# Performance work log

Measured on AMD Instinct MI355X. Metric: run time of the kernel, lower is better.

Reference implementation:

```python
import jax, jax.numpy as jnp
import numpy as np

N = 50000
E = 800000
F = 64
HID = 64
HEADS = 4
NTYPES = 3


def layer_norm(x, g, b, eps=1e-5):
    mu = x.mean(-1, keepdims=True)
    var = ((x - mu) ** 2).mean(-1, keepdims=True)
    return (x - mu) * jax.lax.rsqrt(var + eps) * g + b


def gat_conv(x, src, dst, n, W, att_src, att_dst, bias, concat):
    # PyG GATConv: per-head linear transform, additive attention, segment softmax over dst.
    H, C = att_src.shape
    xp = (x @ W).reshape(n, H, C)                       # [N,H,C]
    a_s = (xp * att_src).sum(-1)                         # [N,H]
    a_d = (xp * att_dst).sum(-1)                         # [N,H]
    e = jax.nn.leaky_relu(a_s[src] + a_d[dst], 0.2)      # [Etot,H]
    m = jax.ops.segment_max(e, dst, num_segments=n)      # stable softmax per target
    ex = jnp.exp(e - m[dst])
    denom = jax.ops.segment_sum(ex, dst, num_segments=n)
    alpha = ex / (denom[dst] + 1e-16)                    # [Etot,H]
    msg = xp[src] * alpha[:, :, None]                    # [Etot,H,C]
    out = jax.ops.segment_sum(msg, dst, num_segments=n)  # [N,H,C]
    out = out.reshape(n, H * C) if concat else out.mean(1)
    return out + bias


def setup_inputs() -> dict:
    key = jax.random.key(0)
    ks = jax.random.split(key, 12)
    f32 = jnp.float32
    return {
        'node_features': jax.random.normal(ks[0], (N, F), f32),
        'node_types': jax.random.randint(ks[1], (N,), 0, NTYPES),
        'edge_index': jax.random.randint(ks[2], (2, E), 0, N),
        'type_emb': jax.random.normal(ks[3], (NTYPES, HID), f32) * 0.02,
        'proj_W': jax.random.normal(ks[4], (F, HID), f32) / np.sqrt(F).astype(np.float32),
        'proj_b': jnp.zeros((HID,), f32),
        'W0': jax.random.normal(ks[5], (HID, HEADS * HID), f32) / np.sqrt(HID).astype(np.float32),
        'att_src0': jax.random.normal(ks[6], (HEADS, HID), f32) * 0.1,
        'att_dst0': jax.random.normal(ks[7], (HEADS, HID), f32) * 0.1,
        'bias0': jnp.zeros((HEADS * HID,), f32),
        'ln0_g': jnp.ones((HEADS * HID,), f32),
        'ln0_b': jnp.zeros((HEADS * HID,), f32),
        'W1': jax.random.normal(ks[8], (HEADS * HID, HEADS * HID), f32) / np.sqrt(HEADS * HID).astype(np.float32),
        'att_src1': jax.random.normal(ks[9], (HEADS, HID), f32) * 0.1,
        'att_dst1': jax.random.normal(ks[10], (HEADS, HID), f32) * 0.1,
        'bias1': jnp.zeros((HID,), f32),
        'ln1_g': jnp.ones((HID,), f32),
        'ln1_b': jnp.zeros((HID,), f32),
    }


def reference(node_features, node_types, edge_index, type_emb, proj_W, proj_b,
              W0, att_src0, att_dst0, bias0, ln0_g, ln0_b,
              W1, att_src1, att_dst1, bias1, ln1_g, ln1_b):
    n = node_features.shape[0]
    loop = jnp.arange(n)
    src = jnp.concatenate([edge_index[0], loop])  # add_self_loops=True (PyG default)
    dst = jnp.concatenate([edge_index[1], loop])
    # input projection + node-type embedding
    x = node_features @ proj_W + proj_b + type_emb[node_types]
    # layer 0: concat heads -> [N, HEADS*HID]
    h = gat_conv(x, src, dst, n, W0, att_src0, att_dst0, bias0, True)
    h = jax.nn.relu(layer_norm(h, ln0_g, ln0_b))  # dropout is identity in eval
    # layer 1: mean over heads -> [N, HID]; residual skipped (shape mismatch 256 vs 64)
    h2 = gat_conv(h, src, dst, n, W1, att_src1, att_dst1, bias1, False)
    h2 = jax.nn.relu(layer_norm(h2, ln1_g, ln1_b))
    return h2
```

## Files before the change

### kernel.cpp

```cpp
#include <hip/hip_runtime.h>
#include <hip/hip_bf16.h>
#include <hip/hip_fp16.h>

typedef unsigned short u16;
typedef unsigned int u32;
typedef short s16x8 __attribute__((ext_vector_type(8)));
typedef float f32x4 __attribute__((ext_vector_type(4)));

__device__ __forceinline__ float bf2f(u16 u) {
  return __uint_as_float(((u32)u) << 16);
}

__device__ __forceinline__ u16 f2b(float f) {
  __hip_bfloat16 h = __float2bfloat16(f);
  return *(u16*)&h;
}

__device__ __forceinline__ u32 packbf(float lo, float hi) {
  return (u32)f2b(lo) | ((u32)f2b(hi) << 16);
}

__device__ __forceinline__ bool sniff_bf16(const void* ones) {
  u32 w = *(const u32*)ones;
  return (w >> 16) == (w & 0xFFFFu);
}

__device__ __forceinline__ float ldf(const void* p, size_t i, bool bf) {
  return bf ? bf2f(((const u16*)p)[i]) : ((const float*)p)[i];
}

__global__ __launch_bounds__(256) void deg_count_k(const int* __restrict__ ei, int E, int N,
                                                   int* __restrict__ deg) {
  int i = blockIdx.x * 256 + threadIdx.x;
  if (i >= E + N) return;
  int d = (i < E) ? ei[E + i] : (i - E);
  atomicAdd(deg + d, 1);
}

__global__ __launch_bounds__(256) void scan_local_k(const int* __restrict__ deg,
                                                    int* __restrict__ off,
                                                    int* __restrict__ bsum, int N) {
  __shared__ int ps[256];
  int t = threadIdx.x;
  int i = blockIdx.x * 256 + t;
  int v = (i < N) ? deg[i] : 0;
  ps[t] = v;
  __syncthreads();
#pragma unroll
  for (int o = 1; o < 256; o <<= 1) {
    int u = (t >= o) ? ps[t - o] : 0;
    __syncthreads();
    ps[t] += u;
    __syncthreads();
  }
  if (i < N) off[i] = ps[t] - v;
  if (t == 255) bsum[blockIdx.x] = ps[255];
}

__global__ __launch_bounds__(256) void scan_add2_k(int* __restrict__ off,
                                                   const int* __restrict__ bsum,
                                                   int* __restrict__ cur,
                                                   int N, int Etot, int nb) {
  __shared__ int red[256];
  int t = threadIdx.x;
  int b = blockIdx.x;
  red[t] = (t < nb && t < b) ? bsum[t] : 0;
  __syncthreads();
#pragma unroll
  for (int o = 128; o > 0; o >>= 1) {
    if (t < o) red[t] += red[t + o];
    __syncthreads();
  }
  int pre = red[0];
  int i = b * 256 + t;
  if (i == 0) off[N] = Etot;
  if (i >= N) return;
  int o2 = off[i] + pre;
  off[i] = o2;
  cur[i] = o2;
}

__global__ __launch_bounds__(256) void scatter_k(const int* __restrict__ ei, int E, int N,
                                                 int* __restrict__ cur, int* __restrict__ csr) {
  int i = blockIdx.x * 256 + threadIdx.x;
  if (i >= E + N) return;
  int s, d;
  if (i < E) { s = ei[i]; d = ei[E + i]; } else { s = i - E; d = s; }
  int p = atomicAdd(cur + d, 1);
  csr[p] = s;
}

__global__ __launch_bounds__(256) void prep_k(
    const void* __restrict__ W0, const void* __restrict__ W1,
    const void* __restrict__ pW, const void* __restrict__ atts,
    const void* __restrict__ attd, const void* __restrict__ pb,
    const void* __restrict__ temb, const void* __restrict__ ones,
    u16* __restrict__ Wp0, u16* __restrict__ Wp1, u16* __restrict__ Wpp,
    u16* __restrict__ Wpe, float* __restrict__ ca) {
  bool bf = sniff_bf16(ones);
  int b = blockIdx.x;
  int t = threadIdx.x;
  if (b < 320) {
    const void* W = (b < 64) ? W0 : W1;
    u16* Wp = (b < 64) ? Wp0 : Wp1;
    int i = (b < 64 ? b : b - 64) * 256 + t;
    int j = i & 7;
    int q = (i >> 3) & 3;
    int c = (i >> 5) & 255;
    int kc = i >> 13;
    int k = kc * 32 + q * 8 + j;
    Wp[i] = f2b(ldf(W, (size_t)k * 256 + c, bf));
  } else if (b < 336) {
    int i = (b - 320) * 256 + t;
    int j = i & 7;
    int q = (i >> 3) & 3;
    int c = (i >> 5) & 63;
    int kc = i >> 11;
    int k = kc * 32 + q * 8 + j;
    Wpp[i] = f2b(ldf(pW, (size_t)k * 64 + c, bf));
  } else {
    __shared__ float va[256], vd[256];
    int h = t >> 6, k = t & 63;
    {
      float s = 0.f, d = 0.f;
      for (int c = 0; c < 64; c++) {
        float w = ldf(W0, (size_t)k * 256 + h * 64 + c, bf);
        s += w * ldf(atts, h * 64 + c, bf);
        d += w * ldf(attd, h * 64 + c, bf);
      }
      va[t] = s;
      vd[t] = d;
    }
    __syncthreads();
    {
      int i = k;
      float wa = 0.f, wd = 0.f;
      for (int kk = 0; kk < 64; kk++) {
        float wv = ldf(pW, (size_t)i * 64 + kk, bf);
        wa += wv * va[h * 64 + kk];
        wd += wv * vd[h * 64 + kk];
      }
      int kc = i >> 5, q = (i >> 3) & 3, j = i & 7;
      Wpe[((kc * 16 + h) * 4 + q) * 8 + j] = f2b(wa);
      Wpe[((kc * 16 + 4 + h) * 4 + q) * 8 + j] = f2b(wd);
    }
    Wpe[256 + t] = 0;
    Wpe[768 + t] = 0;
    if (t < 12) {
      int ty = t >> 2, hh = t & 3;
      float sa = 0.f, sd = 0.f;
      for (int kk = 0; kk < 64; kk++) {
        float bv = ldf(pb, kk, bf) + ldf(temb, ty * 64 + kk, bf);
        sa += bv * va[hh * 64 + kk];
        sd += bv * vd[hh * 64 + kk];
      }
      ca[t] = sa;
      ca[12 + t] = sd;
    }
  }
}

__global__ __launch_bounds__(256) void proj2_k(
    const void* __restrict__ nf, const int* __restrict__ ntype,
    const u16* __restrict__ Wpp, const u16* __restrict__ Wpe,
    const void* __restrict__ pbias, const void* __restrict__ temb,
    const float* __restrict__ ca, const void* __restrict__ ones,
    u16* __restrict__ x, float* __restrict__ aS, float* __restrict__ aD, int N) {
  bool bf = sniff_bf16(ones);
  int t = threadIdx.x;
  int wave = t >> 6, lane = t & 63;
  int r = lane & 15, q = lane >> 4;
  int row0 = blockIdx.x * 16;
  int arow = row0 + r;
  if (arow >= N) arow = N - 1;
  f32x4 xacc = {0.f, 0.f, 0.f, 0.f};
  f32x4 eacc = {0.f, 0.f, 0.f, 0.f};
#pragma unroll
  for (int kc = 0; kc < 2; kc++) {
    s16x8 a;
    if (bf) {
      a = *(const s16x8*)((const u16*)nf + (size_t)arow * 64 + kc * 32 + q * 8);
    } else {
      const float* fp = (const float*)nf + (size_t)arow * 64 + kc * 32 + q * 8;
#pragma unroll
      for (int j = 0; j < 8; j++) a[j] = (short)f2b(fp[j]);
    }
    {
      int c = wave * 16 + r;
      s16x8 b = *(const s16x8*)(Wpp + (((size_t)kc * 64 + c) * 4 + q) * 8);
      xacc = __builtin_amdgcn_mfma_f32_16x16x32_bf16(a, b, xacc, 0, 0, 0);
    }
    if (wave == 3) {
      s16x8 b = *(const s16x8*)(Wpe + (((size_t)kc * 16 + r) * 4 + q) * 8);
      eacc = __builtin_amdgcn_mfma_f32_16x16x32_bf16(a, b, eacc, 0, 0, 0);
    }
  }
#pragma unroll
  for (int rg = 0; rg < 4; rg++) {
    int row = row0 + q * 4 + rg;
    if (row >= N) continue;
    int col = wave * 16 + r;
    int ty = ntype[row];
    float v = xacc[rg] + ldf(pbias, col, bf) + ldf(temb, ty * 64 + col, bf);
    x[(size_t)row * 64 + col] = f2b(v);
    if (wave == 3 && r < 8) {
      if (r < 4) aS[(size_t)row * 4 + r] = eacc[rg] + ca[ty * 4 + r];
      else       aD[(size_t)row * 4 + (r - 4)] = eacc[rg] + ca[12 + ty * 4 + (r - 4)];
    }
  }
}

__global__ __launch_bounds__(256) void agg0_k(
    const int* __restrict__ off, const int* __restrict__ csr,
    const float* __restrict__ aS, const float* __restrict__ aD,
    const u16* __restrict__ x, u16* __restrict__ Ag, int N) {
  __shared__ float wlds[4][64][4];
  int wave = threadIdx.x >> 6;
  int lane = threadIdx.x & 63;
  int n = blockIdx.x * 4 + wave;
  if (n >= N) return;
  int start = off[n], end = off[n + 1];
  float4 ad4 = *(const float4*)(aD + (size_t)n * 4);
  float ad[4] = {ad4.x, ad4.y, ad4.z, ad4.w};
  float den[4] = {0.f, 0.f, 0.f, 0.f};
  int hv = lane >> 5;
  int cl = lane & 31;
  float accL[4] = {0.f, 0.f, 0.f, 0.f};
  float accH[4] = {0.f, 0.f, 0.f, 0.f};
  const char* wbase = (const char*)&wlds[wave][0][0] + hv * 16;
  u32 laneoff = (u32)cl * 4u;

  for (int cs = start; cs < end; cs += 64) {
    int cnt = end - cs; if (cnt > 64) cnt = 64;
    u32 sb = 0;
    float ex0 = 0.f, ex1 = 0.f, ex2 = 0.f, ex3 = 0.f;
    if (lane < cnt) {
      int s = csr[cs + lane];
      sb = (u32)s << 7;
      float4 as4 = *(const float4*)(aS + (size_t)s * 4);
      float v0 = as4.x + ad[0]; v0 = (v0 > 0.f ? v0 : 0.2f * v0) - 3.0f; ex0 = __expf(v0);
      float v1 = as4.y + ad[1]; v1 = (v1 > 0.f ? v1 : 0.2f * v1) - 3.0f; ex1 = __expf(v1);
      float v2 = as4.z + ad[2]; v2 = (v2 > 0.f ? v2 : 0.2f * v2) - 3.0f; ex2 = __expf(v2);
      float v3 = as4.w + ad[3]; v3 = (v3 > 0.f ? v3 : 0.2f * v3) - 3.0f; ex3 = __expf(v3);
      den[0] += ex0; den[1] += ex1; den[2] += ex2; den[3] += ex3;
    }
    *(float4*)&wlds[wave][lane][0] = make_float4(ex0, ex1, ex2, ex3);
#pragma unroll 4
    for (int e = 0; e < cnt; e += 2) {
      u32 so0 = (u32)__builtin_amdgcn_readlane((int)sb, e);
      u32 so1 = (u32)__builtin_amdgcn_readlane((int)sb, e + 1);
      u32 so = hv ? so1 : so0;
      u32 d = *(const u32*)((const char*)x + (so + laneoff));
      float4 w = *(const float4*)(wbase + e * 16);
      float xlo = __uint_as_float(d << 16);
      float xhi = __uint_as_float(d & 0xffff0000u);
      accL[0] += w.x * xlo; accH[0] += w.x * xhi;
      accL[1] += w.y * xlo; accH[1] += w.y * xhi;
      accL[2] += w.z * xlo; accH[2] += w.z * xhi;
      accL[3] += w.w * xlo; accH[3] += w.w * xhi;
    }
  }
#pragma unroll
  for (int h = 0; h < 4; h++) {
#pragma unroll
    for (int o = 32; o > 0; o >>= 1) den[h] += __shfl_xor(den[h], o, 64);
  }
#pragma unroll
  for (int h = 0; h < 4; h++) {
    accL[h] += __shfl_xor(accL[h], 32, 64);
    accH[h] += __shfl_xor(accH[h], 32, 64);
  }
  if (lane < 32) {
    u32* agp = (u32*)Ag + (size_t)n * 128 + lane;
#pragma unroll
    for (int h = 0; h < 4; h++) {
      float inv = 1.f / (den[h] + 1e-16f);
      agp[h * 32] = packbf(accL[h] * inv, accH[h] * inv);
    }
  }
}

__global__ __launch_bounds__(256) void l0g1_k(
    const u16* __restrict__ Ag, const u16* __restrict__ Wp0,
    const void* __restrict__ bias0, const void* __restrict__ g0,
    const void* __restrict__ be0, const u16* __restrict__ Wp1,
    const void* __restrict__ atts, const void* __restrict__ attd,
    const void* __restrict__ ones,
    u16* __restrict__ C, float* __restrict__ aS, float* __restrict__ aD, int N) {
  bool bf = sniff_bf16(ones);
  __shared__ u16 hs[16][264];
  __shared__ float sm_s[4][16], sm_q[4][16];
  int t = threadIdx.x;
  int wave = t >> 6, lane = t & 63;
  int r = lane & 15, q = lane >> 4;
  int row0 = blockIdx.x * 16;
  int arow = row0 + r;
  if (arow >= N) arow = N - 1;
  {
    const u16* ap = Ag + (size_t)arow * 256 + wave * 64 + q * 8;
    f32x4 acc[4] = {{0.f, 0.f, 0.f, 0.f}, {0.f, 0.f, 0.f, 0.f},
                    {0.f, 0.f, 0.f, 0.f}, {0.f, 0.f, 0.f, 0.f}};
#pragma unroll
    for (int kc = 0; kc < 2; kc++) {
      s16x8 a = *(const s16x8*)(ap + kc * 32);
#pragma unroll
      for (int ct = 0; ct < 4; ct++) {
        int c = wave * 64 + ct * 16 + r;
        s16x8 b = *(const s16x8*)(Wp0 + (((size_t)kc * 256 + c) * 4 + q) * 8);
        acc[ct] = __builtin_amdgcn_mfma_f32_16x16x32_bf16(a, b, acc[ct], 0, 0, 0);
      }
    }
    float yv[4][4];
    float s_p[4] = {0.f, 0.f, 0.f, 0.f};
    float q_p[4] = {0.f, 0.f, 0.f, 0.f};
#pragma unroll
    for (int ct = 0; ct < 4; ct++) {
      float bc = ldf(bias0, wave * 64 + ct * 16 + r, bf);
#pragma unroll
      for (int rg = 0; rg < 4; rg++) {
        float y = acc[ct][rg] + bc;
        yv[ct][rg] = y;
        s_p[rg] += y;
        q_p[rg] += y * y;
      }
    }
#pragma unroll
    for (int o = 1; o < 16; o <<= 1) {
#pragma unroll
      for (int rg = 0; rg < 4; rg++) {
        s_p[rg] += __shfl_xor(s_p[rg], o, 64);
        q_p[rg] += __shfl_xor(q_p[rg], o, 64);
      }
    }
    if (r == 0) {
#pragma unroll
      for (int rg = 0; rg < 4; rg++) {
        sm_s[wave][q * 4 + rg] = s_p[rg];
        sm_q[wave][q * 4 + rg] = q_p[rg];
      }
    }
    __syncthreads();
#pragma unroll
    for (int rg = 0; rg < 4; rg++) {
      int lr = q * 4 + rg;
      float mu = (sm_s[0][lr] + sm_s[1][lr] + sm_s[2][lr] + sm_s[3][lr]) * (1.f / 256.f);
      float vq = (sm_q[0][lr] + sm_q[1][lr] + sm_q[2][lr] + sm_q[3][lr]) * (1.f / 256.f) - mu * mu;
      float inv = rsqrtf(vq + 1e-5f);
#pragma unroll
      for (int ct = 0; ct < 4; ct++) {
        int c = wave * 64 + ct * 16 + r;
        float o_ = (yv[ct][rg] - mu) * inv * ldf(g0, c, bf) + ldf(be0, c, bf);
        hs[lr][c] = f2b(fmaxf(o_, 0.f));
      }
    }
  }
  __syncthreads();
  int colw = wave * 64;
  f32x4 acc[4] = {{0.f, 0.f, 0.f, 0.f}, {0.f, 0.f, 0.f, 0.f},
                  {0.f, 0.f, 0.f, 0.f}, {0.f, 0.f, 0.f, 0.f}};
#pragma unroll
  for (int kc = 0; kc < 8; kc++) {
    s16x8 a = *(const s16x8*)&hs[r][kc * 32 + q * 8];
#pragma unroll
    for (int ct = 0; ct < 4; ct++) {
      int c = colw + ct * 16 + r;
      s16x8 b = *(const s16x8*)(Wp1 + (((size_t)kc * 256 + c) * 4 + q) * 8);
      acc[ct] = __builtin_amdgcn_mfma_f32_16x16x32_bf16(a, b, acc[ct], 0, 0, 0);
    }
  }
#pragma unroll
  for (int ct = 0; ct < 4; ct++) {
#pragma unroll
    for (int rg = 0; rg < 4; rg++) {
      int row = row0 + q * 4 + rg;
      if (row < N) C[(size_t)row * 256 + colw + ct * 16 + r] = f2b(acc[ct][rg]);
    }
  }
  float sp[4] = {0.f, 0.f, 0.f, 0.f};
  float dp[4] = {0.f, 0.f, 0.f, 0.f};
#pragma unroll
  for (int ct = 0; ct < 4; ct++) {
    int c = colw + ct * 16 + r;
    float av = ldf(atts, c, bf);
    float dv = ldf(attd, c, bf);
#pragma unroll
    for (int rg = 0; rg < 4; rg++) {
      sp[rg] += acc[ct][rg] * av;
      dp[rg] += acc[ct][rg] * dv;
    }
  }
#pragma unroll
  for (int o = 1; o < 16; o <<= 1) {
#pragma unroll
    for (int rg = 0; rg < 4; rg++) {
      sp[rg] += __shfl_xor(sp[rg], o, 64);
      dp[rg] += __shfl_xor(dp[rg], o, 64);
    }
  }
  if (r == 0) {
#pragma unroll
    for (int rg = 0; rg < 4; rg++) {
      int row = row0 + q * 4 + rg;
      if (row < N) {
        aS[(size_t)row * 4 + wave] = sp[rg];
        aD[(size_t)row * 4 + wave] = dp[rg];
      }
    }
  }
}

__global__ __launch_bounds__(256) void agg1_k(
    const int* __restrict__ off, const int* __restrict__ csr,
    const float* __restrict__ aS, const float* __restrict__ aD,
    const u16* __restrict__ xp,
    const void* __restrict__ bias, const void* __restrict__ g,
    const void* __restrict__ b, void* __restrict__ out, int N) {
  bool bf = sniff_bf16(g);
  __shared__ float wlds[4][64][4];
  int wave = threadIdx.x >> 6;
  int lane = threadIdx.x & 63;
  int n = blockIdx.x * 4 + wave;
  if (n >= N) return;
  int start = off[n], end = off[n + 1];
  float4 ad4 = *(const float4*)(aD + (size_t)n * 4);
  float ad[4] = {ad4.x, ad4.y, ad4.z, ad4.w};
  float den[4] = {0.f, 0.f, 0.f, 0.f};
  float acc[4] = {0.f, 0.f, 0.f, 0.f};
  int hh = lane >> 4;
  const float* wptr = &wlds[wave][0][0] + hh;
  u32 laneoff = (u32)lane * 8u;

  for (int cs = start; cs < end; cs += 64) {
    int cnt = end - cs; if (cnt > 64) cnt = 64;
    u32 sb = 0;
    float ex0 = 0.f, ex1 = 0.f, ex2 = 0.f, ex3 = 0.f;
    if (lane < cnt) {
      int s = csr[cs + lane];
      sb = (u32)s << 9;
      float4 as4 = *(const float4*)(aS + (size_t)s * 4);
      float v0 = as4.x + ad[0]; v0 = (v0 > 0.f ? v0 : 0.2f * v0) - 3.0f; ex0 = __expf(v0);
      float v1 = as4.y + ad[1]; v1 = (v1 > 0.f ? v1 : 0.2f * v1) - 3.0f; ex1 = __expf(v1);
      float v2 = as4.z + ad[2]; v2 = (v2 > 0.f ? v2 : 0.2f * v2) - 3.0f; ex2 = __expf(v2);
      float v3 = as4.w + ad[3]; v3 = (v3 > 0.f ? v3 : 0.2f * v3) - 3.0f; ex3 = __expf(v3);
      den[0] += ex0; den[1] += ex1; den[2] += ex2; den[3] += ex3;
    }
    *(float4*)&wlds[wave][lane][0] = make_float4(ex0, ex1, ex2, ex3);
#pragma unroll 8
    for (int e = 0; e < cnt; e++) {
      u32 so = (u32)__builtin_amdgcn_readlane((int)sb, e);
      uint2 d = *(const uint2*)((const char*)xp + (so + laneoff));
      float w = wptr[e * 4];
      acc[0] += w * __uint_as_float(d.x << 16);
      acc[1] += w * __uint_as_float(d.x & 0xffff0000u);
      acc[2] += w * __uint_as_float(d.y << 16);
      acc[3] += w * __uint_as_float(d.y & 0xffff0000u);
    }
  }
#pragma unroll
  for (int h = 0; h < 4; h++) {
#pragma unroll
    for (int o = 32; o > 0; o >>= 1) den[h] += __shfl_xor(den[h], o, 64);
  }
  float dsel = (hh & 2) ? ((hh & 1) ? den[3] : den[2]) : ((hh & 1) ? den[1] : den[0]);
  float inv = 1.f / (dsel + 1e-16f);
  float p0 = acc[0] * inv, p1 = acc[1] * inv, p2 = acc[2] * inv, p3 = acc[3] * inv;
  p0 += __shfl_xor(p0, 16, 64); p0 += __shfl_xor(p0, 32, 64);
  p1 += __shfl_xor(p1, 16, 64); p1 += __shfl_xor(p1, 32, 64);
  p2 += __shfl_xor(p2, 16, 64); p2 += __shfl_xor(p2, 32, 64);
  p3 += __shfl_xor(p3, 16, 64); p3 += __shfl_xor(p3, 32, 64);
  int cb = (lane & 15) * 4;
  float z0 = 0.25f * p0 + ldf(bias, cb + 0, bf);
  float z1 = 0.25f * p1 + ldf(bias, cb + 1, bf);
  float z2 = 0.25f * p2 + ldf(bias, cb + 2, bf);
  float z3 = 0.25f * p3 + ldf(bias, cb + 3, bf);
  float sum = z0 + z1 + z2 + z3;
  sum += __shfl_xor(sum, 1, 64); sum += __shfl_xor(sum, 2, 64);
  sum += __shfl_xor(sum, 4, 64); sum += __shfl_xor(sum, 8, 64);
  float mu = sum * (1.f / 64.f);
  float d0 = z0 - mu, d1 = z1 - mu, d2 = z2 - mu, d3 = z3 - mu;
  float sq = d0 * d0 + d1 * d1 + d2 * d2 + d3 * d3;
  sq += __shfl_xor(sq, 1, 64); sq += __shfl_xor(sq, 2, 64);
  sq += __shfl_xor(sq, 4, 64); sq += __shfl_xor(sq, 8, 64);
  float invs = rsqrtf(sq * (1.f / 64.f) + 1e-5f);
  float y0 = fmaxf(d0 * invs * ldf(g, cb + 0, bf) + ldf(b, cb + 0, bf), 0.f);
  float y1 = fmaxf(d1 * invs * ldf(g, cb + 1, bf) + ldf(b, cb + 1, bf), 0.f);
  float y2 = fmaxf(d2 * invs * ldf(g, cb + 2, bf) + ldf(b, cb + 2, bf), 0.f);
  float y3 = fmaxf(d3 * invs * ldf(g, cb + 3, bf) + ldf(b, cb + 3, bf), 0.f);
  if (lane < 16) {
    if (bf) {
      u32* o32 = (u32*)out + (size_t)n * 32 + lane * 2;
      o32[0] = packbf(y0, y1);
      o32[1] = packbf(y2, y3);
    } else {
      ((float4*)out)[(size_t)n * 16 + lane] = make_float4(y0, y1, y2, y3);
    }
  }
}

extern "C" void kernel_launch(void* const* d_in, const int* in_sizes, int n_in,
                              void* d_out, int out_size, void* d_ws, size_t ws_size,
                              hipStream_t stream) {
  const void* nf   = d_in[0];
  const int* ntyp  = (const int*)d_in[1];
  const int* ei    = (const int*)d_in[2];
  const void* temb = d_in[3];
  const void* pW   = d_in[4];
  const void* pb   = d_in[5];
  const void* W0   = d_in[6];
  const void* as0  = d_in[7];
  const void* ad0  = d_in[8];
  const void* b0   = d_in[9];
  const void* g0   = d_in[10];
  const void* be0  = d_in[11];
  const void* W1   = d_in[12];
  const void* as1  = d_in[13];
  const void* ad1  = d_in[14];
  const void* b1   = d_in[15];
  const void* g1   = d_in[16];
  const void* be1  = d_in[17];

  int N = in_sizes[0] / 64;
  int E = in_sizes[2] / 2;
  int Etot = E + N;

  u16* Wp0 = (u16*)d_ws;
  u16* Wp1 = Wp0 + 64 * 256;
  u16* Wpp = Wp1 + 256 * 256;
  u16* Wpe = Wpp + 64 * 64;
  u16* xb  = Wpe + 1024;
  u16* Ag  = xb + (size_t)N * 64;
  u16* A   = Ag + (size_t)N * 256;
  float* aS0b = (float*)(A + (size_t)N * 256);
  float* aD0b = aS0b + (size_t)N * 4;
  float* aS1b = aD0b + (size_t)N * 4;
  float* aD1b = aS1b + (size_t)N * 4;
  float* ca = aD1b + (size_t)N * 4;
  int* deg  = (int*)(ca + 32);
  int* off  = deg + N;
  int* csr  = off + N + 1;
  int* bsum = csr + Etot;

  dim3 b256(256);
  int nodeBlocks = (N + 3) / 4;
  int edgeBlocksT = (Etot + 255) / 256;
  int gemmBlocks = (N + 15) / 16;
  int scanBlocks = (N + 255) / 256;

  hipMemsetAsync(deg, 0, (size_t)N * sizeof(int), stream);
  deg_count_k<<<edgeBlocksT, b256, 0, stream>>>(ei, E, N, deg);
  scan_local_k<<<scanBlocks, b256, 0, stream>>>(deg, off, bsum, N);
  scan_add2_k<<<scanBlocks, b256, 0, stream>>>(off, bsum, deg, N, Etot, scanBlocks);
  scatter_k<<<edgeBlocksT, b256, 0, stream>>>(ei, E, N, deg, csr);
  prep_k<<<337, b256, 0, stream>>>(W0, W1, pW, as0, ad0, pb, temb, g0,
                                   Wp0, Wp1, Wpp, Wpe, ca);

  proj2_k<<<gemmBlocks, b256, 0, stream>>>(nf, ntyp, Wpp, Wpe, pb, temb, ca, g0,
                                           xb, aS0b, aD0b, N);
  agg0_k<<<nodeBlocks, b256, 0, stream>>>(off, csr, aS0b, aD0b, xb, Ag, N);
  l0g1_k<<<gemmBlocks, b256, 0, stream>>>(Ag, Wp0, b0, g0, be0, Wp1, as1, ad1, g0,
                                          A, aS1b, aD1b, N);
  agg1_k<<<nodeBlocks, b256, 0, stream>>>(off, csr, aS1b, aD1b, A, b1, g1, be1, d_out, N);
}
```

Measured before the change: 403.4 us.

## Handle self-loops implicitly, batch gather loads, fold layer-1 attention into MFMA

Self-loop edges are dropped from the CSR build and each aggregation kernel adds the self contribution directly from the node's own features and logits. This shrinks the atomic count, scatter and CSR size. The gather loops in both aggregation kernels are restructured into batches that issue all loads before the FMAs, to expose more memory-level parallelism. Layer-1 attention logits now come from precomputed W1·att vectors multiplied by one extra MFMA in a single wave, replacing per-column dot products and shuffle reductions. The risks are bf16 rounding of the folded attention weights and the extra prep block.

```diff
diff --git a/kernel.cpp b/kernel.cpp
--- a/kernel.cpp
+++ b/kernel.cpp
@@ -29,12 +29,11 @@
   return bf ? bf2f(((const u16*)p)[i]) : ((const float*)p)[i];
 }
 
-__global__ __launch_bounds__(256) void deg_count_k(const int* __restrict__ ei, int E, int N,
+__global__ __launch_bounds__(256) void deg_count_k(const int* __restrict__ ei, int E,
                                                    int* __restrict__ deg) {
   int i = blockIdx.x * 256 + threadIdx.x;
-  if (i >= E + N) return;
-  int d = (i < E) ? ei[E + i] : (i - E);
-  atomicAdd(deg + d, 1);
+  if (i >= E) return;
+  atomicAdd(deg + ei[E + i], 1);
 }
 
 __global__ __launch_bounds__(256) void scan_local_k(const int* __restrict__ deg,
@@ -80,12 +79,11 @@
   cur[i] = o2;
 }
 
-__global__ __launch_bounds__(256) void scatter_k(const int* __restrict__ ei, int E, int N,
+__global__ __launch_bounds__(256) void scatter_k(const int* __restrict__ ei, int E,
                                                  int* __restrict__ cur, int* __restrict__ csr) {
   int i = blockIdx.x * 256 + threadIdx.x;
-  if (i >= E + N) return;
-  int s, d;
-  if (i < E) { s = ei[i]; d = ei[E + i]; } else { s = i - E; d = s; }
+  if (i >= E) return;
+  int s = ei[i], d = ei[E + i];
   int p = atomicAdd(cur + d, 1);
   csr[p] = s;
 }
@@ -93,10 +91,11 @@
 __global__ __launch_bounds__(256) void prep_k(
     const void* __restrict__ W0, const void* __restrict__ W1,
     const void* __restrict__ pW, const void* __restrict__ atts,
-    const void* __restrict__ attd, const void* __restrict__ pb,
+    const void* __restrict__ attd, const void* __restrict__ as1,
+    const void* __restrict__ ad1, const void* __restrict__ pb,
     const void* __restrict__ temb, const void* __restrict__ ones,
     u16* __restrict__ Wp0, u16* __restrict__ Wp1, u16* __restrict__ Wpp,
-    u16* __restrict__ Wpe, float* __restrict__ ca) {
+    u16* __restrict__ Wpe, u16* __restrict__ Wpe1, float* __restrict__ ca) {
   bool bf = sniff_bf16(ones);
   int b = blockIdx.x;
   int t = threadIdx.x;
@@ -118,7 +117,7 @@
     int kc = i >> 11;
     int k = kc * 32 + q * 8 + j;
     Wpp[i] = f2b(ldf(pW, (size_t)k * 64 + c, bf));
-  } else {
+  } else if (b == 336) {
     __shared__ float va[256], vd[256];
     int h = t >> 6, k = t & 63;
     {
@@ -156,6 +155,28 @@
       }
       ca[t] = sa;
       ca[12 + t] = sd;
+    }
+  } else {
+    int k = t;
+    for (int z = t; z < 4096; z += 256) Wpe1[z] = 0;
+    __syncthreads();
+    float sa[4], sd[4];
+#pragma unroll
+    for (int h = 0; h < 4; h++) {
+      float a_ = 0.f, d_ = 0.f;
+      for (int j = 0; j < 64; j++) {
+        float wv = ldf(W1, (size_t)k * 256 + h * 64 + j, bf);
+        a_ += wv * ldf(as1, h * 64 + j, bf);
+        d_ += wv * ldf(ad1, h * 64 + j, bf);
+      }
+      sa[h] = a_;
+      sd[h] = d_;
+    }
+    int kc = k >> 5, q = (k >> 3) & 3, j = k & 7;
+#pragma unroll
+    for (int h = 0; h < 4; h++) {
+      Wpe1[((kc * 16 + h) * 4 + q) * 8 + j] = f2b(sa[h]);
+      Wpe1[((kc * 16 + 4 + h) * 4 + q) * 8 + j] = f2b(sd[h]);
     }
   }
 }
@@ -222,6 +243,7 @@
   int start = off[n], end = off[n + 1];
   float4 ad4 = *(const float4*)(aD + (size_t)n * 4);
   float ad[4] = {ad4.x, ad4.y, ad4.z, ad4.w};
+  float4 sad = *(const float4*)(aS + (size_t)n * 4);
   float den[4] = {0.f, 0.f, 0.f, 0.f};
   int hv = lane >> 5;
   int cl = lane & 31;
@@ -229,6 +251,40 @@
   float accH[4] = {0.f, 0.f, 0.f, 0.f};
   const char* wbase = (const char*)&wlds[wave][0][0] + hv * 16;
   u32 laneoff = (u32)cl * 4u;
+
+  float exs[4];
+  {
+    float sv[4] = {sad.x, sad.y, sad.z, sad.w};
+#pragma unroll
+    for (int h = 0; h < 4; h++) {
+      float v = sv[h] + ad[h];
+      v = (v > 0.f ? v : 0.2f * v) - 3.0f;
+      exs[h] = __expf(v);
+    }
+  }
+
+#define AGG0_BATCH(P)                                                            \
+  {                                                                              \
+    u32 dd[P];                                                                   \
+    float4 w[P];                                                                 \
+    _Pragma("unroll") for (int j = 0; j < P; j++) {                              \
+      u32 so0 = (u32)__builtin_amdgcn_readlane((int)sb, e + 2 * j);              \
+      u32 so1 = (u32)__builtin_amdgcn_readlane((int)sb, e + 2 * j + 1);          \
+      u32 so = hv ? so1 : so0;                                                   \
+      dd[j] = *(const u32*)((const char*)x + (so + laneoff));                    \
+    }                                                                            \
+    _Pragma("unroll") for (int j = 0; j < P; j++) {                              \
+      w[j] = *(const float4*)(wbase + (e + 2 * j) * 16);                         \
+    }                                                                            \
+    _Pragma("unroll") for (int j = 0; j < P; j++) {                              \
+      float xlo = __uint_as_float(dd[j] << 16);                                  \
+      float xhi = __uint_as_float(dd[j] & 0xffff0000u);                          \
+      accL[0] += w[j].x * xlo; accH[0] += w[j].x * xhi;                          \
+      accL[1] += w[j].y * xlo; accH[1] += w[j].y * xhi;                          \
+      accL[2] += w[j].z * xlo; accH[2] += w[j].z * xhi;                          \
+      accL[3] += w[j].w * xlo; accH[3] += w[j].w * xhi;                          \
+    }                                                                            \
+  }
 
   for (int cs = start; cs < end; cs += 64) {
     int cnt = end - cs; if (cnt > 64) cnt = 64;
@@ -245,25 +301,31 @@
       den[0] += ex0; den[1] += ex1; den[2] += ex2; den[3] += ex3;
     }
     *(float4*)&wlds[wave][lane][0] = make_float4(ex0, ex1, ex2, ex3);
-#pragma unroll 4
-    for (int e = 0; e < cnt; e += 2) {
-      u32 so0 = (u32)__builtin_amdgcn_readlane((int)sb, e);
-      u32 so1 = (u32)__builtin_amdgcn_readlane((int)sb, e + 1);
-      u32 so = hv ? so1 : so0;
-      u32 d = *(const u32*)((const char*)x + (so + laneoff));
-      float4 w = *(const float4*)(wbase + e * 16);
-      float xlo = __uint_as_float(d << 16);
-      float xhi = __uint_as_float(d & 0xffff0000u);
-      accL[0] += w.x * xlo; accH[0] += w.x * xhi;
-      accL[1] += w.y * xlo; accH[1] += w.y * xhi;
-      accL[2] += w.z * xlo; accH[2] += w.z * xhi;
-      accL[3] += w.w * xlo; accH[3] += w.w * xhi;
-    }
+    int e = 0;
+    int full = cnt & ~15;
+    for (; e < full; e += 16) AGG0_BATCH(8)
+    int rem = cnt - e;
+    if (rem > 0) {
+      if (rem <= 8) AGG0_BATCH(4)
+      else          AGG0_BATCH(8)
+    }
+  }
+#undef AGG0_BATCH
+  {
+    u32 dself = *(const u32*)((const char*)x + (((u32)n << 7) + laneoff));
+    float s0 = __uint_as_float(dself << 16);
+    float s1 = __uint_as_float(dself & 0xffff0000u);
+    float ws[4];
+#pragma unroll
+    for (int h = 0; h < 4; h++) ws[h] = hv ? 0.f : exs[h];
+#pragma unroll
+    for (int h = 0; h < 4; h++) { accL[h] += ws[h] * s0; accH[h] += ws[h] * s1; }
   }
 #pragma unroll
   for (int h = 0; h < 4; h++) {
 #pragma unroll
     for (int o = 32; o > 0; o >>= 1) den[h] += __shfl_xor(den[h], o, 64);
+    den[h] += exs[h];
   }
 #pragma unroll
   for (int h = 0; h < 4; h++) {
@@ -284,8 +346,7 @@
     const u16* __restrict__ Ag, const u16* __restrict__ Wp0,
     const void* __restrict__ bias0, const void* __restrict__ g0,
     const void* __restrict__ be0, const u16* __restrict__ Wp1,
-    const void* __restrict__ atts, const void* __restrict__ attd,
-    const void* __restrict__ ones,
+    const u16* __restrict__ Wpe1, const void* __restrict__ ones,
     u16* __restrict__ C, float* __restrict__ aS, float* __restrict__ aD, int N) {
   bool bf = sniff_bf16(ones);
   __shared__ u16 hs[16][264];
@@ -358,6 +419,7 @@
   int colw = wave * 64;
   f32x4 acc[4] = {{0.f, 0.f, 0.f, 0.f}, {0.f, 0.f, 0.f, 0.f},
                   {0.f, 0.f, 0.f, 0.f}, {0.f, 0.f, 0.f, 0.f}};
+  f32x4 eacc = {0.f, 0.f, 0.f, 0.f};
 #pragma unroll
   for (int kc = 0; kc < 8; kc++) {
     s16x8 a = *(const s16x8*)&hs[r][kc * 32 + q * 8];
@@ -367,6 +429,10 @@
       s16x8 b = *(const s16x8*)(Wp1 + (((size_t)kc * 256 + c) * 4 + q) * 8);
       acc[ct] = __builtin_amdgcn_mfma_f32_16x16x32_bf16(a, b, acc[ct], 0, 0, 0);
     }
+    if (wave == 3) {
+      s16x8 be = *(const s16x8*)(Wpe1 + (((size_t)kc * 16 + r) * 4 + q) * 8);
+      eacc = __builtin_amdgcn_mfma_f32_16x16x32_bf16(a, be, eacc, 0, 0, 0);
+    }
   }
 #pragma unroll
   for (int ct = 0; ct < 4; ct++) {
@@ -376,34 +442,13 @@
       if (row < N) C[(size_t)row * 256 + colw + ct * 16 + r] = f2b(acc[ct][rg]);
     }
   }
-  float sp[4] = {0.f, 0.f, 0.f, 0.f};
-  float dp[4] = {0.f, 0.f, 0.f, 0.f};
-#pragma unroll
-  for (int ct = 0; ct < 4; ct++) {
-    int c = colw + ct * 16 + r;
-    float av = ldf(atts, c, bf);
-    float dv = ldf(attd, c, bf);
-#pragma unroll
-    for (int rg = 0; rg < 4; rg++) {
-      sp[rg] += acc[ct][rg] * av;
-      dp[rg] += acc[ct][rg] * dv;
-    }
-  }
-#pragma unroll
-  for (int o = 1; o < 16; o <<= 1) {
-#pragma unroll
-    for (int rg = 0; rg < 4; rg++) {
-      sp[rg] += __shfl_xor(sp[rg], o, 64);
-      dp[rg] += __shfl_xor(dp[rg], o, 64);
-    }
-  }
-  if (r == 0) {
+  if (wave == 3 && r < 8) {
 #pragma unroll
     for (int rg = 0; rg < 4; rg++) {
       int row = row0 + q * 4 + rg;
       if (row < N) {
-        aS[(size_t)row * 4 + wave] = sp[rg];
-        aD[(size_t)row * 4 + wave] = dp[rg];
+        if (r < 4) aS[(size_t)row * 4 + r] = eacc[rg];
+        else       aD[(size_t)row * 4 + (r - 4)] = eacc[rg];
       }
     }
   }
@@ -424,11 +469,40 @@
   int start = off[n], end = off[n + 1];
   float4 ad4 = *(const float4*)(aD + (size_t)n * 4);
   float ad[4] = {ad4.x, ad4.y, ad4.z, ad4.w};
+  float4 sad = *(const float4*)(aS + (size_t)n * 4);
   float den[4] = {0.f, 0.f, 0.f, 0.f};
   float acc[4] = {0.f, 0.f, 0.f, 0.f};
   int hh = lane >> 4;
   const float* wptr = &wlds[wave][0][0] + hh;
   u32 laneoff = (u32)lane * 8u;
+
+  float exs[4];
+  {
+    float sv[4] = {sad.x, sad.y, sad.z, sad.w};
+#pragma unroll
+    for (int h = 0; h < 4; h++) {
+      float v = sv[h] + ad[h];
+      v = (v > 0.f ? v : 0.2f * v) - 3.0f;
+      exs[h] = __expf(v);
+    }
+  }
+
+#define AGG1_BATCH(K)                                                            \
+  {                                                                              \
+    uint2 d[K];                                                                  \
+    float w[K];                                                                  \
+    _Pragma("unroll") for (int j = 0; j < K; j++) {                              \
+      u32 so = (u32)__builtin_amdgcn_readlane((int)sb, e + j);                   \
+      d[j] = *(const uint2*)((const char*)xp + (so + laneoff));                  \
+    }                                                                            \
+    _Pragma("unroll") for (int j = 0; j < K; j++) w[j] = wptr[(e + j) * 4];      \
+    _Pragma("unroll") for (int j = 0; j < K; j++) {                              \
+      acc[0] += w[j] * __uint_as_float(d[j].x << 16);                            \
+      acc[1] += w[j] * __uint_as_float(d[j].x & 0xffff0000u);                    \
+      acc[2] += w[j] * __uint_as_float(d[j].y << 16);                            \
+      acc[3] += w[j] * __uint_as_float(d[j].y & 0xffff0000u);                    \
+    }                                                                            \
+  }
 
   for (int cs = start; cs < end; cs += 64) {
     int cnt = end - cs; if (cnt > 64) cnt = 64;
@@ -445,21 +519,29 @@
       den[0] += ex0; den[1] += ex1; den[2] += ex2; den[3] += ex3;
     }
     *(float4*)&wlds[wave][lane][0] = make_float4(ex0, ex1, ex2, ex3);
-#pragma unroll 8
-    for (int e = 0; e < cnt; e++) {
-      u32 so = (u32)__builtin_amdgcn_readlane((int)sb, e);
-      uint2 d = *(const uint2*)((const char*)xp + (so + laneoff));
-      float w = wptr[e * 4];
-      acc[0] += w * __uint_as_float(d.x << 16);
-      acc[1] += w * __uint_as_float(d.x & 0xffff0000u);
-      acc[2] += w * __uint_as_float(d.y << 16);
-      acc[3] += w * __uint_as_float(d.y & 0xffff0000u);
-    }
+    int e = 0;
+    int full = cnt & ~7;
+    for (; e < full; e += 8) AGG1_BATCH(8)
+    int rem = cnt - e;
+    if (rem > 0) {
+      if (rem <= 4) AGG1_BATCH(4)
+      else          AGG1_BATCH(8)
+    }
+  }
+#undef AGG1_BATCH
+  {
+    uint2 ds_ = *(const uint2*)((const char*)xp + (((u32)n << 9) + laneoff));
+    float wsel = (hh & 2) ? ((hh & 1) ? exs[3] : exs[2]) : ((hh & 1) ? exs[1] : exs[0]);
+    acc[0] += wsel * __uint_as_float(ds_.x << 16);
+    acc[1] += wsel * __uint_as_float(ds_.x & 0xffff0000u);
+    acc[2] += wsel * __uint_as_float(ds_.y << 16);
+    acc[3] += wsel * __uint_as_float(ds_.y & 0xffff0000u);
   }
 #pragma unroll
   for (int h = 0; h < 4; h++) {
 #pragma unroll
     for (int o = 32; o > 0; o >>= 1) den[h] += __shfl_xor(den[h], o, 64);
+    den[h] += exs[h];
   }
   float dsel = (hh & 2) ? ((hh & 1) ? den[3] : den[2]) : ((hh & 1) ? den[1] : den[0]);
   float inv = 1.f / (dsel + 1e-16f);
@@ -521,13 +603,13 @@
 
   int N = in_sizes[0] / 64;
   int E = in_sizes[2] / 2;
-  int Etot = E + N;
 
   u16* Wp0 = (u16*)d_ws;
   u16* Wp1 = Wp0 + 64 * 256;
   u16* Wpp = Wp1 + 256 * 256;
   u16* Wpe = Wpp + 64 * 64;
-  u16* xb  = Wpe + 1024;
+  u16* Wpe1 = Wpe + 1024;
+  u16* xb  = Wpe1 + 4096;
   u16* Ag  = xb + (size_t)N * 64;
   u16* A   = Ag + (size_t)N * 256;
   float* aS0b = (float*)(A + (size_t)N * 256);
@@ -538,26 +620,26 @@
   int* deg  = (int*)(ca + 32);
   int* off  = deg + N;
   int* csr  = off + N + 1;
-  int* bsum = csr + Etot;
+  int* bsum = csr + E;
 
   dim3 b256(256);
   int nodeBlocks = (N + 3) / 4;
-  int edgeBlocksT = (Etot + 255) / 256;
+  int edgeBlocks = (E + 255) / 256;
   int gemmBlocks = (N + 15) / 16;
   int scanBlocks = (N + 255) / 256;
 
   hipMemsetAsync(deg, 0, (size_t)N * sizeof(int), stream);
-  deg_count_k<<<edgeBlocksT, b256, 0, stream>>>(ei, E, N, deg);
+  deg_count_k<<<edgeBlocks, b256, 0, stream>>>(ei, E, deg);
   scan_local_k<<<scanBlocks, b256, 0, stream>>>(deg, off, bsum, N);
-  scan_add2_k<<<scanBlocks, b256, 0, stream>>>(off, bsum, deg, N, Etot, scanBlocks);
-  scatter_k<<<edgeBlocksT, b256, 0, stream>>>(ei, E, N, deg, csr);
-  prep_k<<<337, b256, 0, stream>>>(W0, W1, pW, as0, ad0, pb, temb, g0,
-                                   Wp0, Wp1, Wpp, Wpe, ca);
+  scan_add2_k<<<scanBlocks, b256, 0, stream>>>(off, bsum, deg, N, E, scanBlocks);
+  scatter_k<<<edgeBlocks, b256, 0, stream>>>(ei, E, deg, csr);
+  prep_k<<<338, b256, 0, stream>>>(W0, W1, pW, as0, ad0, as1, ad1, pb, temb, g0,
+                                   Wp0, Wp1, Wpp, Wpe, Wpe1, ca);
 
   proj2_k<<<gemmBlocks, b256, 0, stream>>>(nf, ntyp, Wpp, Wpe, pb, temb, ca, g0,
                                            xb, aS0b, aD0b, N);
   agg0_k<<<nodeBlocks, b256, 0, stream>>>(off, csr, aS0b, aD0b, xb, Ag, N);
-  l0g1_k<<<gemmBlocks, b256, 0, stream>>>(Ag, Wp0, b0, g0, be0, Wp1, as1, ad1, g0,
+  l0g1_k<<<gemmBlocks, b256, 0, stream>>>(Ag, Wp0, b0, g0, be0, Wp1, Wpe1, g0,
                                           A, aS1b, aD1b, N);
   agg1_k<<<nodeBlocks, b256, 0, stream>>>(off, csr, aS1b, aD1b, A, b1, g1, be1, d_out, N);
 }
```

After: 414.2 us. +2.7%, slower.

## Double-buffer gather loads in aggregation kernels and fold layer-1 attention into MFMA

Applied to the files above, without the earlier changes.

Both edge-aggregation kernels now issue batches of eight gathered neighbour loads into one register buffer while consuming the previous batch from the other. This keeps more memory requests in flight and hides gather latency. Separately, the layer-1 attention logits are computed with an extra MFMA against precomputed W1·att vectors built in a new prep block, replacing the per-column dot products and cross-lane shuffle reductions. The cost is higher register pressure, which may lower occupancy, and padded tail iterations that read zeroed LDS weights.

```diff
diff --git a/kernel.cpp b/kernel.cpp
--- a/kernel.cpp
+++ b/kernel.cpp
@@ -93,10 +93,11 @@
 __global__ __launch_bounds__(256) void prep_k(
     const void* __restrict__ W0, const void* __restrict__ W1,
     const void* __restrict__ pW, const void* __restrict__ atts,
-    const void* __restrict__ attd, const void* __restrict__ pb,
+    const void* __restrict__ attd, const void* __restrict__ as1,
+    const void* __restrict__ ad1, const void* __restrict__ pb,
     const void* __restrict__ temb, const void* __restrict__ ones,
     u16* __restrict__ Wp0, u16* __restrict__ Wp1, u16* __restrict__ Wpp,
-    u16* __restrict__ Wpe, float* __restrict__ ca) {
+    u16* __restrict__ Wpe, u16* __restrict__ Wpe1, float* __restrict__ ca) {
   bool bf = sniff_bf16(ones);
   int b = blockIdx.x;
   int t = threadIdx.x;
@@ -118,7 +119,7 @@
     int kc = i >> 11;
     int k = kc * 32 + q * 8 + j;
     Wpp[i] = f2b(ldf(pW, (size_t)k * 64 + c, bf));
-  } else {
+  } else if (b == 336) {
     __shared__ float va[256], vd[256];
     int h = t >> 6, k = t & 63;
     {
@@ -156,6 +157,28 @@
       }
       ca[t] = sa;
       ca[12 + t] = sd;
+    }
+  } else {
+    int k = t;
+    for (int z = t; z < 4096; z += 256) Wpe1[z] = 0;
+    __syncthreads();
+    float sa[4], sd[4];
+#pragma unroll
+    for (int h = 0; h < 4; h++) {
+      float a_ = 0.f, d_ = 0.f;
+      for (int j = 0; j < 64; j++) {
+        float wv = ldf(W1, (size_t)k * 256 + h * 64 + j, bf);
+        a_ += wv * ldf(as1, h * 64 + j, bf);
+        d_ += wv * ldf(ad1, h * 64 + j, bf);
+      }
+      sa[h] = a_;
+      sd[h] = d_;
+    }
+    int kc = k >> 5, q = (k >> 3) & 3, j = k & 7;
+#pragma unroll
+    for (int h = 0; h < 4; h++) {
+      Wpe1[((kc * 16 + h) * 4 + q) * 8 + j] = f2b(sa[h]);
+      Wpe1[((kc * 16 + 4 + h) * 4 + q) * 8 + j] = f2b(sd[h]);
     }
   }
 }
@@ -230,6 +253,28 @@
   const char* wbase = (const char*)&wlds[wave][0][0] + hv * 16;
   u32 laneoff = (u32)cl * 4u;
 
+#define AGG0_ISSUE(D, base)                                                      \
+  _Pragma("unroll") for (int j = 0; j < 8; j++) {                                \
+    u32 so0 = (u32)__builtin_amdgcn_readlane((int)sb, (base) + 2 * j);           \
+    u32 so1 = (u32)__builtin_amdgcn_readlane((int)sb, (base) + 2 * j + 1);       \
+    u32 so = hv ? so1 : so0;                                                     \
+    D[j] = *(const u32*)((const char*)x + (so + laneoff));                       \
+  }
+#define AGG0_CONS(D, base)                                                       \
+  {                                                                              \
+    float4 w[8];                                                                 \
+    _Pragma("unroll") for (int j = 0; j < 8; j++)                                \
+      w[j] = *(const float4*)(wbase + ((base) + 2 * j) * 16);                    \
+    _Pragma("unroll") for (int j = 0; j < 8; j++) {                              \
+      float xlo = __uint_as_float(D[j] << 16);                                   \
+      float xhi = __uint_as_float(D[j] & 0xffff0000u);                           \
+      accL[0] += w[j].x * xlo; accH[0] += w[j].x * xhi;                          \
+      accL[1] += w[j].y * xlo; accH[1] += w[j].y * xhi;                          \
+      accL[2] += w[j].z * xlo; accH[2] += w[j].z * xhi;                          \
+      accL[3] += w[j].w * xlo; accH[3] += w[j].w * xhi;                          \
+    }                                                                            \
+  }
+
   for (int cs = start; cs < end; cs += 64) {
     int cnt = end - cs; if (cnt > 64) cnt = 64;
     u32 sb = 0;
@@ -245,21 +290,22 @@
       den[0] += ex0; den[1] += ex1; den[2] += ex2; den[3] += ex3;
     }
     *(float4*)&wlds[wave][lane][0] = make_float4(ex0, ex1, ex2, ex3);
-#pragma unroll 4
-    for (int e = 0; e < cnt; e += 2) {
-      u32 so0 = (u32)__builtin_amdgcn_readlane((int)sb, e);
-      u32 so1 = (u32)__builtin_amdgcn_readlane((int)sb, e + 1);
-      u32 so = hv ? so1 : so0;
-      u32 d = *(const u32*)((const char*)x + (so + laneoff));
-      float4 w = *(const float4*)(wbase + e * 16);
-      float xlo = __uint_as_float(d << 16);
-      float xhi = __uint_as_float(d & 0xffff0000u);
-      accL[0] += w.x * xlo; accH[0] += w.x * xhi;
-      accL[1] += w.y * xlo; accH[1] += w.y * xhi;
-      accL[2] += w.z * xlo; accH[2] += w.z * xhi;
-      accL[3] += w.w * xlo; accH[3] += w.w * xhi;
-    }
-  }
+    int cnt16 = (cnt + 15) & ~15;
+    int nb = cnt16 >> 4;
+    u32 d0[8], d1[8];
+    AGG0_ISSUE(d0, 0)
+    for (int bi = 1; bi < nb; bi++) {
+      int base = bi << 4;
+      if (bi & 1) { AGG0_ISSUE(d1, base) AGG0_CONS(d0, base - 16) }
+      else        { AGG0_ISSUE(d0, base) AGG0_CONS(d1, base - 16) }
+    }
+    {
+      int lb = (nb - 1) << 4;
+      if (nb & 1) { AGG0_CONS(d0, lb) } else { AGG0_CONS(d1, lb) }
+    }
+  }
+#undef AGG0_ISSUE
+#undef AGG0_CONS
 #pragma unroll
   for (int h = 0; h < 4; h++) {
 #pragma unroll
@@ -284,8 +330,7 @@
     const u16* __restrict__ Ag, const u16* __restrict__ Wp0,
     const void* __restrict__ bias0, const void* __restrict__ g0,
     const void* __restrict__ be0, const u16* __restrict__ Wp1,
-    const void* __restrict__ atts, const void* __restrict__ attd,
-    const void* __restrict__ ones,
+    const u16* __restrict__ Wpe1, const void* __restrict__ ones,
     u16* __restrict__ C, float* __restrict__ aS, float* __restrict__ aD, int N) {
   bool bf = sniff_bf16(ones);
   __shared__ u16 hs[16][264];
@@ -358,6 +403,7 @@
   int colw = wave * 64;
   f32x4 acc[4] = {{0.f, 0.f, 0.f, 0.f}, {0.f, 0.f, 0.f, 0.f},
                   {0.f, 0.f, 0.f, 0.f}, {0.f, 0.f, 0.f, 0.f}};
+  f32x4 eacc = {0.f, 0.f, 0.f, 0.f};
 #pragma unroll
   for (int kc = 0; kc < 8; kc++) {
     s16x8 a = *(const s16x8*)&hs[r][kc * 32 + q * 8];
@@ -367,6 +413,10 @@
       s16x8 b = *(const s16x8*)(Wp1 + (((size_t)kc * 256 + c) * 4 + q) * 8);
       acc[ct] = __builtin_amdgcn_mfma_f32_16x16x32_bf16(a, b, acc[ct], 0, 0, 0);
     }
+    if (wave == 3) {
+      s16x8 be = *(const s16x8*)(Wpe1 + (((size_t)kc * 16 + r) * 4 + q) * 8);
+      eacc = __builtin_amdgcn_mfma_f32_16x16x32_bf16(a, be, eacc, 0, 0, 0);
+    }
   }
 #pragma unroll
   for (int ct = 0; ct < 4; ct++) {
@@ -376,34 +426,13 @@
       if (row < N) C[(size_t)row * 256 + colw + ct * 16 + r] = f2b(acc[ct][rg]);
     }
   }
-  float sp[4] = {0.f, 0.f, 0.f, 0.f};
-  float dp[4] = {0.f, 0.f, 0.f, 0.f};
-#pragma unroll
-  for (int ct = 0; ct < 4; ct++) {
-    int c = colw + ct * 16 + r;
-    float av = ldf(atts, c, bf);
-    float dv = ldf(attd, c, bf);
-#pragma unroll
-    for (int rg = 0; rg < 4; rg++) {
-      sp[rg] += acc[ct][rg] * av;
-      dp[rg] += acc[ct][rg] * dv;
-    }
-  }
-#pragma unroll
-  for (int o = 1; o < 16; o <<= 1) {
-#pragma unroll
-    for (int rg = 0; rg < 4; rg++) {
-      sp[rg] += __shfl_xor(sp[rg], o, 64);
-      dp[rg] += __shfl_xor(dp[rg], o, 64);
-    }
-  }
-  if (r == 0) {
+  if (wave == 3 && r < 8) {
 #pragma unroll
     for (int rg = 0; rg < 4; rg++) {
       int row = row0 + q * 4 + rg;
       if (row < N) {
-        aS[(size_t)row * 4 + wave] = sp[rg];
-        aD[(size_t)row * 4 + wave] = dp[rg];
+        if (r < 4) aS[(size_t)row * 4 + r] = eacc[rg];
+        else       aD[(size_t)row * 4 + (r - 4)] = eacc[rg];
       }
     }
   }
@@ -430,6 +459,23 @@
   const float* wptr = &wlds[wave][0][0] + hh;
   u32 laneoff = (u32)lane * 8u;
 
+#define AGG1_ISSUE(D, base)                                                      \
+  _Pragma("unroll") for (int j = 0; j < 8; j++) {                                \
+    u32 so = (u32)__builtin_amdgcn_readlane((int)sb, (base) + j);                \
+    D[j] = *(const uint2*)((const char*)xp + (so + laneoff));                    \
+  }
+#define AGG1_CONS(D, base)                                                       \
+  {                                                                              \
+    float w[8];                                                                  \
+    _Pragma("unroll") for (int j = 0; j < 8; j++) w[j] = wptr[((base) + j) * 4]; \
+    _Pragma("unroll") for (int j = 0; j < 8; j++) {                              \
+      acc[0] += w[j] * __uint_as_float(D[j].x << 16);                            \
+      acc[1] += w[j] * __uint_as_float(D[j].x & 0xffff0000u);                    \
+      acc[2] += w[j] * __uint_as_float(D[j].y << 16);                            \
+      acc[3] += w[j] * __uint_as_float(D[j].y & 0xffff0000u);                    \
+    }                                                                            \
+  }
+
   for (int cs = start; cs < end; cs += 64) {
     int cnt = end - cs; if (cnt > 64) cnt = 64;
     u32 sb = 0;
@@ -445,17 +491,22 @@
       den[0] += ex0; den[1] += ex1; den[2] += ex2; den[3] += ex3;
     }
     *(float4*)&wlds[wave][lane][0] = make_float4(ex0, ex1, ex2, ex3);
-#pragma unroll 8
-    for (int e = 0; e < cnt; e++) {
-      u32 so = (u32)__builtin_amdgcn_readlane((int)sb, e);
-      uint2 d = *(const uint2*)((const char*)xp + (so + laneoff));
-      float w = wptr[e * 4];
-      acc[0] += w * __uint_as_float(d.x << 16);
-      acc[1] += w * __uint_as_float(d.x & 0xffff0000u);
-      acc[2] += w * __uint_as_float(d.y << 16);
-      acc[3] += w * __uint_as_float(d.y & 0xffff0000u);
-    }
-  }
+    int cnt8 = (cnt + 7) & ~7;
+    int nb = cnt8 >> 3;
+    uint2 d0[8], d1[8];
+    AGG1_ISSUE(d0, 0)
+    for (int bi = 1; bi < nb; bi++) {
+      int base = bi << 3;
+      if (bi & 1) { AGG1_ISSUE(d1, base) AGG1_CONS(d0, base - 8) }
+      else        { AGG1_ISSUE(d0, base) AGG1_CONS(d1, base - 8) }
+    }
+    {
+      int lb = (nb - 1) << 3;
+      if (nb & 1) { AGG1_CONS(d0, lb) } else { AGG1_CONS(d1, lb) }
+    }
+  }
+#undef AGG1_ISSUE
+#undef AGG1_CONS
 #pragma unroll
   for (int h = 0; h < 4; h++) {
 #pragma unroll
@@ -527,7 +578,8 @@
   u16* Wp1 = Wp0 + 64 * 256;
   u16* Wpp = Wp1 + 256 * 256;
   u16* Wpe = Wpp + 64 * 64;
-  u16* xb  = Wpe + 1024;
+  u16* Wpe1 = Wpe + 1024;
+  u16* xb  = Wpe1 + 4096;
   u16* Ag  = xb + (size_t)N * 64;
   u16* A   = Ag + (size_t)N * 256;
   float* aS0b = (float*)(A + (size_t)N * 256);
@@ -551,13 +603,13 @@
   scan_local_k<<<scanBlocks, b256, 0, stream>>>(deg, off, bsum, N);
   scan_add2_k<<<scanBlocks, b256, 0, stream>>>(off, bsum, deg, N, Etot, scanBlocks);
   scatter_k<<<edgeBlocksT, b256, 0, stream>>>(ei, E, N, deg, csr);
-  prep_k<<<337, b256, 0, stream>>>(W0, W1, pW, as0, ad0, pb, temb, g0,
-                                   Wp0, Wp1, Wpp, Wpe, ca);
+  prep_k<<<338, b256, 0, stream>>>(W0, W1, pW, as0, ad0, as1, ad1, pb, temb, g0,
+                                   Wp0, Wp1, Wpp, Wpe, Wpe1, ca);
 
   proj2_k<<<gemmBlocks, b256, 0, stream>>>(nf, ntyp, Wpp, Wpe, pb, temb, ca, g0,
                                            xb, aS0b, aD0b, N);
   agg0_k<<<nodeBlocks, b256, 0, stream>>>(off, csr, aS0b, aD0b, xb, Ag, N);
-  l0g1_k<<<gemmBlocks, b256, 0, stream>>>(Ag, Wp0, b0, g0, be0, Wp1, as1, ad1, g0,
+  l0g1_k<<<gemmBlocks, b256, 0, stream>>>(Ag, Wp0, b0, g0, be0, Wp1, Wpe1, g0,
                                           A, aS1b, aD1b, N);
   agg1_k<<<nodeBlocks, b256, 0, stream>>>(off, csr, aS1b, aD1b, A, b1, g1, be1, d_out, N);
 }
```

Measured after the change: 409.0 us. Within noise of the previous version (+1.4%).
